# Optimization experiments

Measured on AMD Instinct MI355X. Metric: run time of the kernel, lower is better.

The kernel has to match this reference:

```python
import jax, jax.numpy as jnp
import numpy as np

D_MODEL = 1024
NUM_HEADS = 4
KEY_DIM = 1024      # expand_k = 1
VALUE_DIM = 2048    # expand_v = 2
HEAD_QK = KEY_DIM // NUM_HEADS   # 256
HEAD_V = VALUE_DIM // NUM_HEADS  # 512
EPS = 1e-5
CHUNK = 64
ROPE_BASE = 10000.0


def apply_rotary(q, k):
    # q, k: (b, n, h, d), non-interleaved (rotate-half) rotary
    n, d = q.shape[1], q.shape[-1]
    inv_freq = 1.0 / (ROPE_BASE ** (jnp.arange(0, d, 2, dtype=jnp.float32) / d))
    t = jnp.arange(n, dtype=jnp.float32)
    freqs = jnp.outer(t, inv_freq)                     # (n, d/2)
    cos = jnp.cos(freqs)[None, :, None, :]
    sin = jnp.sin(freqs)[None, :, None, :]
    def rot(x):
        x1, x2 = jnp.split(x, 2, axis=-1)
        return jnp.concatenate([x1 * cos - x2 * sin, x2 * cos + x1 * sin], axis=-1)
    return rot(q), rot(k)


def chunk_retention(q, k, v, gamma, chunk=CHUNK):
    # q,k: (B,H,N,dk); v: (B,H,N,dv); gamma: (H,) per-head decay
    B, H, N, dk = q.shape
    dv = v.shape[-1]
    NC = N // chunk
    # (NC, B, H, C, d) chunked layout for scan
    qc = jnp.moveaxis(q.reshape(B, H, NC, chunk, dk), 2, 0)
    kc = jnp.moveaxis(k.reshape(B, H, NC, chunk, dk), 2, 0)
    vc = jnp.moveaxis(v.reshape(B, H, NC, chunk, dv), 2, 0)

    idx = jnp.arange(chunk)
    rel = idx[:, None] - idx[None, :]                       # i - j
    # intra-chunk decay mask D[h,i,j] = gamma_h**(i-j) for i>=j else 0
    D = jnp.where(rel >= 0, gamma[:, None, None] ** rel, 0.0)       # (H,C,C)
    cross_q = (gamma[:, None] ** (idx + 1))[None, :, :, None]       # (1,H,C,1)
    cross_k = (gamma[:, None] ** (chunk - 1 - idx))[None, :, :, None]
    gC = (gamma ** chunk)[None, :, None, None]                      # (1,H,1,1)

    def step(S, qkv):
        qb, kb, vb = qkv                                    # (B,H,C,d)
        attn = jnp.einsum('bhid,bhjd->bhij', qb, kb) * D[None]
        o_intra = jnp.einsum('bhij,bhjd->bhid', attn, vb)
        o_inter = jnp.einsum('bhid,bhde->bhie', qb * cross_q, S)
        S_new = gC * S + jnp.einsum('bhjd,bhje->bhde', kb * cross_k, vb)
        return S_new, o_intra + o_inter

    S0 = jnp.zeros((B, H, dk, dv), dtype=q.dtype)
    _, o = jax.lax.scan(step, S0, (qc, kc, vc))             # (NC,B,H,C,dv)
    return jnp.moveaxis(o, 0, 2).reshape(B, H, N, dv)


def rmsnorm(x, w):
    var = jnp.mean(x * x, axis=-1, keepdims=True)
    return x * jax.lax.rsqrt(var + EPS) * w


def setup_inputs() -> dict:
    key = jax.random.key(0)
    ks = jax.random.split(key, 7)
    B, N = 2, 4096
    s = 0.02
    return {
        'x': jax.random.normal(ks[0], (B, N, D_MODEL), dtype=jnp.float32),
        'Wq': jax.random.normal(ks[1], (D_MODEL, D_MODEL), dtype=jnp.float32) * s,
        'Wk': jax.random.normal(ks[2], (D_MODEL, D_MODEL), dtype=jnp.float32) * s,
        'Wv': jax.random.normal(ks[3], (D_MODEL, VALUE_DIM), dtype=jnp.float32) * s,
        'Wg': jax.random.normal(ks[4], (D_MODEL, VALUE_DIM), dtype=jnp.float32) * s,
        'Wo': jax.random.normal(ks[5], (VALUE_DIM, D_MODEL), dtype=jnp.float32) * s,
        'gn_weight': jnp.ones((HEAD_V,), dtype=jnp.float32),
    }


def reference(x, Wq, Wk, Wv, Wg, Wo, gn_weight):
    B, N, _ = x.shape
    H = NUM_HEADS
    q1 = (x @ Wq).reshape(B, N, H, HEAD_QK)
    k1 = (x @ Wk).reshape(B, N, H, HEAD_QK)
    q1, k1 = apply_rotary(q1, k1)
    q = jnp.transpose(q1, (0, 2, 1, 3)) * (HEAD_QK ** -0.5)   # (B,H,N,dk)
    k = jnp.transpose(k1, (0, 2, 1, 3))
    v = jnp.transpose((x @ Wv).reshape(B, N, H, HEAD_V), (0, 2, 1, 3))
    gamma = 1.0 - jnp.exp2(-5.0 - jnp.arange(H, dtype=jnp.float32))
    o = chunk_retention(q, k, v, gamma)                       # (B,H,N,dv_h)
    o = jnp.transpose(o, (0, 2, 1, 3))                        # (B,N,H,dv_h)
    o = rmsnorm(o, gn_weight)
    g = jax.nn.silu(x @ Wg)                                   # (B,N,VALUE_DIM)
    o = o.reshape(B, N, VALUE_DIM) * g
    return o @ Wo
```

## Files before the change

kernel.cpp:

```cpp
#include <hip/hip_runtime.h>

#define NS   4096
#define NBAT 2
#define NH   4
#define DKH  256
#define DVH  512
#define DM   1024
#define VD   2048
#define CH   64
#define NCH  64
#define MROW (NBAT * NS)

typedef unsigned short u16;
typedef unsigned int   u32;

using bf16x8 = __attribute__((ext_vector_type(8))) short;
using bf16x4 = __attribute__((ext_vector_type(4))) short;
using f32x4  = __attribute__((ext_vector_type(4))) float;

__device__ __forceinline__ float bf2f(u16 a) {
  return __uint_as_float(((u32)a) << 16);
}
__device__ __forceinline__ u16 f2bf(float f) {
  u32 u = __float_as_uint(f);
  u32 r = (u + 0x7fffu + ((u >> 16) & 1u)) >> 16;
  return (u16)r;
}
__device__ __forceinline__ void unpack2(u32 v, float& lo, float& hi) {
  lo = __uint_as_float(v << 16);
  hi = __uint_as_float(v & 0xffff0000u);
}
__device__ __forceinline__ void unpack8(uint4 v, float* f) {
  unpack2(v.x, f[0], f[1]); unpack2(v.y, f[2], f[3]);
  unpack2(v.z, f[4], f[5]); unpack2(v.w, f[6], f[7]);
}

__device__ __forceinline__ void gl_lds16(const u16* g, u16* l) {
  __builtin_amdgcn_global_load_lds(
      (const __attribute__((address_space(1))) void*)g,
      (__attribute__((address_space(3))) void*)l,
      16, 0, 0);
}

__device__ __forceinline__ f32x4 mfma32(bf16x8 a, bf16x8 b, f32x4 c) {
  return __builtin_amdgcn_mfma_f32_16x16x32_bf16(a, b, c, 0, 0, 0);
}

__device__ __forceinline__ f32x4 mfma16(bf16x4 a, bf16x4 b, f32x4 c) {
#if __has_builtin(__builtin_amdgcn_mfma_f32_16x16x16bf16_1k)
  return __builtin_amdgcn_mfma_f32_16x16x16bf16_1k(a, b, c, 0, 0, 0);
#else
  asm("v_mfma_f32_16x16x16_bf16 %0, %1, %2, %0" : "+v"(c) : "v"(a), "v"(b));
  return c;
#endif
}

__device__ __forceinline__ bf16x8 scale8(bf16x8 v, const float* ckv) {
  u32* w = (u32*)&v;
  bf16x8 out;
  u32* ow = (u32*)&out;
#pragma unroll
  for (int p = 0; p < 4; p++) {
    float lo, hi; unpack2(w[p], lo, hi);
    ow[p] = (u32)f2bf(lo * ckv[2 * p]) | ((u32)f2bf(hi * ckv[2 * p + 1]) << 16);
  }
  return out;
}

__device__ __forceinline__ bf16x4 pack4(f32x4 v) {
  bf16x4 o;
  o[0] = (short)f2bf(v[0]); o[1] = (short)f2bf(v[1]);
  o[2] = (short)f2bf(v[2]); o[3] = (short)f2bf(v[3]);
  return o;
}

__global__ __launch_bounds__(256) void cvt_bf16(const float* __restrict__ X,
                                                u16* __restrict__ Y) {
  size_t t = (size_t)blockIdx.x * 256 + threadIdx.x;
  float4 v = *(const float4*)(X + t * 4);
  ushort4 o;
  o.x = f2bf(v.x); o.y = f2bf(v.y); o.z = f2bf(v.z); o.w = f2bf(v.w);
  *(ushort4*)(Y + t * 4) = o;
}

__global__ __launch_bounds__(256) void transpose_bf16(const float* __restrict__ W,
                                                      u16* __restrict__ Wt,
                                                      int K, int N) {
  __shared__ float tile[64][65];
  const int n0 = blockIdx.x * 64, k0 = blockIdx.y * 64;
  const int t = threadIdx.x;
  const int r = t >> 4, c = (t & 15) << 2;
#pragma unroll
  for (int it = 0; it < 4; it++) {
    float4 v = *(const float4*)(W + (size_t)(k0 + r + it * 16) * N + n0 + c);
    tile[r + it * 16][c + 0] = v.x; tile[r + it * 16][c + 1] = v.y;
    tile[r + it * 16][c + 2] = v.z; tile[r + it * 16][c + 3] = v.w;
  }
  __syncthreads();
#pragma unroll
  for (int it = 0; it < 4; it++) {
    const int nr = r + it * 16;
    ushort4 o;
    o.x = f2bf(tile[c + 0][nr]); o.y = f2bf(tile[c + 1][nr]);
    o.z = f2bf(tile[c + 2][nr]); o.w = f2bf(tile[c + 3][nr]);
    *(ushort4*)(Wt + (size_t)(n0 + nr) * K + k0 + c) = o;
  }
}

template<int OMODE>
__global__ __launch_bounds__(256) void gemm_mfma(const u16* __restrict__ A,
                                                 const u16* __restrict__ Bt,
                                                 void* __restrict__ C,
                                                 int M, int N, int K) {
  __shared__ u16 sA[128 * 64];
  __shared__ u16 sB[128 * 64];
  const int tid = threadIdx.x;
  const int wave = tid >> 6, lane = tid & 63;
  const int wm = (wave >> 1) << 6;
  const int wn = (wave & 1) << 6;
  const int row0 = blockIdx.y << 7, col0 = blockIdx.x << 7;

  const int srow = tid >> 3;
  const int sk   = (tid & 7) << 3;

  const u16* aRow = A + (size_t)(row0 + srow) * K + sk;
  const u16* bRow = Bt + (size_t)(col0 + srow) * K + sk;
  u16* sAp = sA + tid * 8;
  u16* sBp = sB + tid * 8;

  f32x4 acc[4][4] = {};

  const int fm = lane & 15;
  const int fk = (lane >> 4) << 3;
  const u16* sAf = sA + (wm + fm) * 64 + fk;
  const u16* sBf = sB + (wn + fm) * 64 + fk;

  for (int k0 = 0; k0 < K; k0 += 64) {
#pragma unroll
    for (int it = 0; it < 4; it++) {
      gl_lds16(aRow + (size_t)(it * 32) * K + k0, sAp + it * 2048);
      gl_lds16(bRow + (size_t)(it * 32) * K + k0, sBp + it * 2048);
    }
    __syncthreads();
#pragma unroll
    for (int kk = 0; kk < 64; kk += 32) {
      bf16x8 af[4], bfr[4];
#pragma unroll
      for (int mt = 0; mt < 4; mt++) af[mt] = *(const bf16x8*)(sAf + mt * 1024 + kk);
#pragma unroll
      for (int nt = 0; nt < 4; nt++) bfr[nt] = *(const bf16x8*)(sBf + nt * 1024 + kk);
#pragma unroll
      for (int mt = 0; mt < 4; mt++)
#pragma unroll
        for (int nt = 0; nt < 4; nt++)
          acc[mt][nt] = mfma32(af[mt], bfr[nt], acc[mt][nt]);
    }
    __syncthreads();
  }

  const int er = lane >> 4;
  const int ec = lane & 15;
#pragma unroll
  for (int mt = 0; mt < 4; mt++) {
#pragma unroll
    for (int nt = 0; nt < 4; nt++) {
      if constexpr (OMODE == 2) {
        ushort4 o;
        o.x = f2bf(acc[mt][nt][0]); o.y = f2bf(acc[mt][nt][1]);
        o.z = f2bf(acc[mt][nt][2]); o.w = f2bf(acc[mt][nt][3]);
        u16* dst = (u16*)C + (size_t)(col0 + wn + nt * 16 + ec) * M +
                   row0 + wm + mt * 16 + er * 4;
        *(ushort4*)dst = o;
      } else {
#pragma unroll
        for (int r = 0; r < 4; r++) {
          const size_t row = (size_t)row0 + wm + mt * 16 + er * 4 + r;
          const size_t col = (size_t)col0 + wn + nt * 16 + ec;
          if constexpr (OMODE == 1) ((u16*)C)[row * N + col] = f2bf(acc[mt][nt][r]);
          else                      ((float*)C)[row * N + col] = acc[mt][nt][r];
        }
      }
    }
  }
}

__global__ __launch_bounds__(256) void rope_kernel(u16* __restrict__ Q, u16* __restrict__ K) {
  size_t t = (size_t)blockIdx.x * 256 + threadIdx.x;
  int j = (int)(t & 127);
  int h = (int)((t >> 7) & 3);
  size_t bn = t >> 9;
  int n = (int)(bn & (NS - 1));
  float ang = (float)n * exp2f(-(float)j * (13.2877123795494f / 128.0f));
  float s, c;
  sincosf(ang, &s, &c);
  size_t base = bn * DM + (size_t)h * DKH + j;
  const float sc = 0.0625f;
  float q1 = bf2f(Q[base]), q2 = bf2f(Q[base + 128]);
  Q[base]       = f2bf((q1 * c - q2 * s) * sc);
  Q[base + 128] = f2bf((q2 * c + q1 * s) * sc);
  float k1 = bf2f(K[base]), k2 = bf2f(K[base + 128]);
  K[base]       = f2bf(k1 * c - k2 * s);
  K[base + 128] = f2bf(k2 * c + k1 * s);
}

__global__ __launch_bounds__(256) void transpose_k(const u16* __restrict__ Kb,
                                                   u16* __restrict__ KT) {
  __shared__ u16 tile[64][68];
  const int wg = blockIdx.x;
  const int dt = wg & 3, nt = (wg >> 2) & 63, h = (wg >> 8) & 3, b = wg >> 10;
  const int tid = threadIdx.x;
  const int r = tid >> 2, cb = (tid & 3) << 4;
  const u16* src = Kb + (size_t)(b * NS + nt * 64 + r) * DM + h * DKH + dt * 64 + cb;
  *(uint4*)&tile[r][cb]     = *(const uint4*)(src);
  *(uint4*)&tile[r][cb + 8] = *(const uint4*)(src + 8);
  __syncthreads();
  const int dr = tid >> 2, ncb = (tid & 3) << 4;
  u32 w[8];
#pragma unroll
  for (int u = 0; u < 8; u++)
    w[u] = (u32)tile[ncb + 2 * u][dr] | ((u32)tile[ncb + 2 * u + 1][dr] << 16);
  u16* dst = KT + ((size_t)((b * NH + h) * 256) + dt * 64 + dr) * NS + nt * 64 + ncb;
  *(uint4*)(dst)     = make_uint4(w[0], w[1], w[2], w[3]);
  *(uint4*)(dst + 8) = make_uint4(w[4], w[5], w[6], w[7]);
}

__global__ __launch_bounds__(256) void attn_mfma(const u16* __restrict__ Q,
                                                 const u16* __restrict__ Kb,
                                                 u16* __restrict__ At) {
  __shared__ u16 sQ[64][264];
  __shared__ u16 sK[64][264];
  const int wg = blockIdx.x;
  const int c = wg & 63, h = (wg >> 6) & 3, b = wg >> 8;
  const int n0 = c << 6;
  const int tid = threadIdx.x;
  const int wave = tid >> 6, lane = tid & 63;
  const int quad = lane >> 4, col = lane & 15;
  {
    const int r = tid >> 2, cb = (tid & 3) << 6;
    const u16* qsrc = Q  + (size_t)(b * NS + n0 + r) * DM + h * DKH + cb;
    const u16* ksrc = Kb + (size_t)(b * NS + n0 + r) * DM + h * DKH + cb;
#pragma unroll
    for (int u = 0; u < 8; u++) {
      *(uint4*)&sQ[r][cb + u * 8] = *(const uint4*)(qsrc + u * 8);
      *(uint4*)&sK[r][cb + u * 8] = *(const uint4*)(ksrc + u * 8);
    }
  }
  __syncthreads();
  const int i0 = wave << 4;
  f32x4 acc[4] = {};
#pragma unroll
  for (int ks = 0; ks < 256; ks += 32) {
    bf16x8 a = *(const bf16x8*)&sQ[i0 + col][ks + quad * 8];
#pragma unroll
    for (int nt = 0; nt < 4; nt++) {
      bf16x8 bb = *(const bf16x8*)&sK[nt * 16 + col][ks + quad * 8];
      acc[nt] = mfma32(a, bb, acc[nt]);
    }
  }
  const float l2g = log2f(1.0f - exp2f(-5.0f - (float)h));
  u16* dst = At + ((size_t)wg << 12);
#pragma unroll
  for (int nt = 0; nt < 4; nt++) {
    int j = nt * 16 + col;
#pragma unroll
    for (int rr = 0; rr < 4; rr++) {
      int i = i0 + quad * 4 + rr;
      int rel = i - j;
      float v = (rel >= 0) ? acc[nt][rr] * exp2f((float)rel * l2g) : 0.0f;
      dst[i * 64 + j] = f2bf(v);
    }
  }
}

__global__ __launch_bounds__(64) void state_pass(const u16* __restrict__ KT,
                                                 const u16* __restrict__ VT,
                                                 u16* __restrict__ Sc) {
  const int wg = blockIdx.x;
  const int bh = wg & 7, slice = wg >> 3;
  const int ds = slice & 7, es = slice >> 3;
  const int b = bh >> 2, h = bh & 3;
  const int lane = threadIdx.x;
  const int quad = lane >> 4, col = lane & 15;
  const float gamma = 1.0f - exp2f(-5.0f - (float)h);
  const float l2g = log2f(gamma);
  const float gC = exp2f(64.0f * l2g);
  float ck[2][8];
#pragma unroll
  for (int ks = 0; ks < 2; ks++)
#pragma unroll
    for (int u = 0; u < 8; u++)
      ck[ks][u] = exp2f((float)(63 - (ks * 32 + quad * 8 + u)) * l2g);

  const u16* KTb = KT + (size_t)(bh * 256 + ds * 32) * NS;
  const u16* vrow = VT + (size_t)(h * DVH + es * 16 + col) * MROW + (size_t)b * NS;

  f32x4 S[2] = {};
  bf16x8 kf[2][4], vf[2][2];

#pragma unroll
  for (int mt = 0; mt < 2; mt++)
#pragma unroll
    for (int ks = 0; ks < 2; ks++)
      kf[0][mt * 2 + ks] = *(const bf16x8*)(KTb + (size_t)(mt * 16 + col) * NS + ks * 32 + quad * 8);
#pragma unroll
  for (int ks = 0; ks < 2; ks++)
    vf[0][ks] = *(const bf16x8*)(vrow + ks * 32 + quad * 8);

#pragma unroll 2
  for (int ch = 0; ch < NCH; ch++) {
    const int cur = ch & 1, nxt = cur ^ 1;
    if (ch + 1 < NCH) {
      const int n1 = (ch + 1) << 6;
#pragma unroll
      for (int mt = 0; mt < 2; mt++)
#pragma unroll
        for (int ks = 0; ks < 2; ks++)
          kf[nxt][mt * 2 + ks] = *(const bf16x8*)(KTb + (size_t)(mt * 16 + col) * NS + n1 + ks * 32 + quad * 8);
#pragma unroll
      for (int ks = 0; ks < 2; ks++)
        vf[nxt][ks] = *(const bf16x8*)(vrow + n1 + ks * 32 + quad * 8);
    }
#pragma unroll
    for (int mt = 0; mt < 2; mt++) S[mt] *= gC;
#pragma unroll
    for (int ks = 0; ks < 2; ks++) {
      bf16x8 ckv = scale8(vf[cur][ks], ck[ks]);
#pragma unroll
      for (int mt = 0; mt < 2; mt++)
        S[mt] = mfma32(kf[cur][mt * 2 + ks], ckv, S[mt]);
    }
    if ((ch & 7) == 7 && ch != NCH - 1) {
      const int sidx = ch >> 3;
      u16* sp = Sc + (size_t)((bh * 7 + sidx) * 512 + es * 16 + col) * 256 + ds * 32;
#pragma unroll
      for (int mt = 0; mt < 2; mt++) {
        ushort4 o;
        o.x = f2bf(S[mt][0]); o.y = f2bf(S[mt][1]);
        o.z = f2bf(S[mt][2]); o.w = f2bf(S[mt][3]);
        *(ushort4*)(sp + mt * 16 + quad * 4) = o;
      }
    }
  }
}

__global__ __launch_bounds__(64, 1) void out_pass(const u16* __restrict__ Q,
                                                  const u16* __restrict__ KT,
                                                  const u16* __restrict__ At,
                                                  const u16* __restrict__ VT,
                                                  const u16* __restrict__ Sc,
                                                  u16* __restrict__ O) {
  const int wg = blockIdx.x;
  const int grp = wg & 63, es = wg >> 6;
  const int sc = grp & 7, bh = grp >> 3;
  const int b = bh >> 2, h = bh & 3;
  const int lane = threadIdx.x;
  const int quad = lane >> 4, col = lane & 15;
  const float gamma = 1.0f - exp2f(-5.0f - (float)h);
  const float l2g = log2f(gamma);
  const float gC = exp2f(64.0f * l2g);
  const float g16 = exp2f(16.0f * l2g);
  const float cq00 = exp2f((float)(quad * 4 + 1) * l2g);
  float ck[2][8];
#pragma unroll
  for (int ks = 0; ks < 2; ks++)
#pragma unroll
    for (int u = 0; u < 8; u++)
      ck[ks][u] = exp2f((float)(63 - (ks * 32 + quad * 8 + u)) * l2g);

  const u16* Qb  = Q + (size_t)(b * NS) * DM + h * DKH;
  const u16* KTb = KT + (size_t)(bh * 256) * NS;
  const u16* Atb = At + ((size_t)(bh * NCH) << 12);
  const u16* vrow0 = VT + (size_t)(h * DVH + es * 32 + col) * MROW + (size_t)b * NS;
  const u16* vrow1 = vrow0 + (size_t)16 * MROW;
  u16* Ob = O + (size_t)(b * NS) * VD + h * DVH + es * 32;

  f32x4 S[2][16];
  bf16x4 SB[2][16];
  if (sc) {
    const u16* sp0 = Sc + (size_t)((bh * 7 + sc - 1) * 512 + es * 32 + col) * 256;
    const u16* sp1 = sp0 + (size_t)16 * 256;
#pragma unroll
    for (int mt = 0; mt < 16; mt++) {
      ushort4 w0 = *(const ushort4*)(sp0 + mt * 16 + quad * 4);
      ushort4 w1 = *(const ushort4*)(sp1 + mt * 16 + quad * 4);
      SB[0][mt][0] = (short)w0.x; SB[0][mt][1] = (short)w0.y;
      SB[0][mt][2] = (short)w0.z; SB[0][mt][3] = (short)w0.w;
      SB[1][mt][0] = (short)w1.x; SB[1][mt][1] = (short)w1.y;
      SB[1][mt][2] = (short)w1.z; SB[1][mt][3] = (short)w1.w;
      S[0][mt] = f32x4{bf2f(w0.x), bf2f(w0.y), bf2f(w0.z), bf2f(w0.w)};
      S[1][mt] = f32x4{bf2f(w1.x), bf2f(w1.y), bf2f(w1.z), bf2f(w1.w)};
    }
  } else {
#pragma unroll
    for (int nt = 0; nt < 2; nt++)
#pragma unroll
      for (int mt = 0; mt < 16; mt++) { S[nt][mt] = f32x4{0.f, 0.f, 0.f, 0.f}; SB[nt][mt] = bf16x4{0, 0, 0, 0}; }
  }

  for (int c = 0; c < 8; c++) {
    const int ch = sc * 8 + c;
    const int n0 = ch << 6;
    f32x4 ai[4][2] = {}, ae[4][2] = {};
    bf16x8 vfr[2][2];
#pragma unroll
    for (int ks = 0; ks < 2; ks++) {
      vfr[ks][0] = *(const bf16x8*)(vrow0 + n0 + ks * 32 + quad * 8);
      vfr[ks][1] = *(const bf16x8*)(vrow1 + n0 + ks * 32 + quad * 8);
#pragma unroll
      for (int mt = 0; mt < 4; mt++) {
        bf16x8 a = *(const bf16x8*)(Atb + ((size_t)ch << 12) + (mt * 16 + col) * 64 + ks * 32 + quad * 8);
        ai[mt][0] = mfma32(a, vfr[ks][0], ai[mt][0]);
        ai[mt][1] = mfma32(a, vfr[ks][1], ai[mt][1]);
      }
    }
    if (sc || c) {
#pragma unroll
      for (int kt = 0; kt < 16; kt++) {
#pragma unroll
        for (int mt = 0; mt < 4; mt++) {
          ushort4 qa = *(const ushort4*)(Qb + (size_t)(n0 + mt * 16 + col) * DM + kt * 16 + quad * 4);
          bf16x4 a; a[0] = (short)qa.x; a[1] = (short)qa.y; a[2] = (short)qa.z; a[3] = (short)qa.w;
          ae[mt][0] = mfma16(a, SB[0][kt], ae[mt][0]);
          ae[mt][1] = mfma16(a, SB[1][kt], ae[mt][1]);
        }
      }
    }
    float cqr = cq00;
#pragma unroll
    for (int mt = 0; mt < 4; mt++) {
      float cq = cqr;
#pragma unroll
      for (int r = 0; r < 4; r++) {
        u16* dst = Ob + (size_t)(n0 + mt * 16 + quad * 4 + r) * VD;
        dst[col]      = f2bf(ai[mt][0][r] + cq * ae[mt][0][r]);
        dst[16 + col] = f2bf(ai[mt][1][r] + cq * ae[mt][1][r]);
        cq *= gamma;
      }
      cqr *= g16;
    }
    if (c < 7) {
#pragma unroll
      for (int nt = 0; nt < 2; nt++)
#pragma unroll
        for (int mt = 0; mt < 16; mt++) S[nt][mt] *= gC;
#pragma unroll
      for (int ks = 0; ks < 2; ks++) {
        bf16x8 ckv0 = scale8(vfr[ks][0], ck[ks]);
        bf16x8 ckv1 = scale8(vfr[ks][1], ck[ks]);
#pragma unroll
        for (int mt = 0; mt < 16; mt++) {
          bf16x8 a = *(const bf16x8*)(KTb + (size_t)(mt * 16 + col) * NS + n0 + ks * 32 + quad * 8);
          S[0][mt] = mfma32(a, ckv0, S[0][mt]);
          S[1][mt] = mfma32(a, ckv1, S[1][mt]);
        }
      }
#pragma unroll
      for (int nt = 0; nt < 2; nt++)
#pragma unroll
        for (int mt = 0; mt < 16; mt++) SB[nt][mt] = pack4(S[nt][mt]);
    }
  }
}

__global__ __launch_bounds__(256) void norm_gate_kernel(const u16* __restrict__ O,
                                                        const u16* __restrict__ G,
                                                        const float* __restrict__ gnw,
                                                        u16* __restrict__ OG) {
  const int bn = blockIdx.x;
  const int wave = threadIdx.x >> 6;
  const int lane = threadIdx.x & 63;
  const size_t base = (size_t)bn * VD + (size_t)wave * DVH;
  float vals[8];
  float ss = 0.f;
#pragma unroll
  for (int k = 0; k < 8; k++) {
    float v = bf2f(O[base + lane + 64 * k]);
    vals[k] = v;
    ss += v * v;
  }
#pragma unroll
  for (int off = 32; off > 0; off >>= 1) ss += __shfl_xor(ss, off, 64);
  const float r = rsqrtf(ss * (1.0f / 512.0f) + 1e-5f);
#pragma unroll
  for (int k = 0; k < 8; k++) {
    int e = lane + 64 * k;
    float g = bf2f(G[base + e]);
    float sig = 1.0f / (1.0f + expf(-g));
    OG[base + e] = f2bf(vals[k] * r * gnw[e] * g * sig);
  }
}

extern "C" void kernel_launch(void* const* d_in, const int* in_sizes, int n_in,
                              void* d_out, int out_size, void* d_ws, size_t ws_size,
                              hipStream_t stream) {
  const float* x   = (const float*)d_in[0];
  const float* Wq  = (const float*)d_in[1];
  const float* Wk  = (const float*)d_in[2];
  const float* Wv  = (const float*)d_in[3];
  const float* Wg  = (const float*)d_in[4];
  const float* Wo  = (const float*)d_in[5];
  const float* gnw = (const float*)d_in[6];

  char* ws = (char*)d_ws;
  u16*   xb  = (u16*)(ws);
  u16*   Sc  = (u16*)(ws);
  u16*   Qb  = (u16*)(ws + (16u  << 20));
  u16*   Kb  = (u16*)(ws + (32u  << 20));
  u16*   VT  = (u16*)(ws + (48u  << 20));
  u16*   Gb  = (u16*)(ws + (80u  << 20));
  u16*   At  = (u16*)(ws + (112u << 20));
  u16*   KTg = (u16*)(ws + (116u << 20));
  u16*   Wqt = (u16*)(ws + (132u << 20));
  u16*   Wkt = (u16*)(ws + (134u << 20));
  u16*   Wvt = (u16*)(ws + (136u << 20));
  u16*   Wgt = (u16*)(ws + (140u << 20));
  u16*   Wot = (u16*)(ws + (144u << 20));
  u16*   Ob  = (u16*)(ws + (148u << 20));
  u16*   OG  = (u16*)(ws);

  dim3 blk(256);
  const int M = MROW;

  cvt_bf16<<<8192, blk, 0, stream>>>(x, xb);
  transpose_bf16<<<dim3(16, 16), blk, 0, stream>>>(Wq, Wqt, DM, DM);
  transpose_bf16<<<dim3(16, 16), blk, 0, stream>>>(Wk, Wkt, DM, DM);
  transpose_bf16<<<dim3(32, 16), blk, 0, stream>>>(Wv, Wvt, DM, VD);
  transpose_bf16<<<dim3(32, 16), blk, 0, stream>>>(Wg, Wgt, DM, VD);
  transpose_bf16<<<dim3(16, 32), blk, 0, stream>>>(Wo, Wot, VD, DM);

  gemm_mfma<1><<<dim3(8, 64),  blk, 0, stream>>>(xb, Wqt, Qb, M, DM, DM);
  gemm_mfma<1><<<dim3(8, 64),  blk, 0, stream>>>(xb, Wkt, Kb, M, DM, DM);
  gemm_mfma<2><<<dim3(16, 64), blk, 0, stream>>>(xb, Wvt, VT, M, VD, DM);
  gemm_mfma<1><<<dim3(16, 64), blk, 0, stream>>>(xb, Wgt, Gb, M, VD, DM);

  rope_kernel<<<16384, blk, 0, stream>>>(Qb, Kb);
  transpose_k<<<2048, blk, 0, stream>>>(Kb, KTg);
  attn_mfma<<<512, blk, 0, stream>>>(Qb, Kb, At);

  state_pass<<<2048, dim3(64), 0, stream>>>(KTg, VT, Sc);
  out_pass<<<1024, dim3(64), 0, stream>>>(Qb, KTg, At, VT, Sc, Ob);

  norm_gate_kernel<<<M, blk, 0, stream>>>(Ob, Gb, gnw, OG);
  gemm_mfma<0><<<dim3(8, 64), blk, 0, stream>>>(OG, Wot, (float*)d_out, M, DM, VD);
}
```

Baseline: 668.8 us.

## Restructure out_pass to 4-wave blocks with LDS-staged state and K=32 MFMA

out_pass now runs 256-thread blocks where each wave owns a 16-column slice of the value dimension instead of 32 columns. The per-wave state operand is staged through LDS as bf16 so the inter-chunk product can use the 16x16x32 MFMA with 8-wide loads, replacing the 16x16x16 instruction and halving the register-resident state. state_pass also stops eight chunks early, since only the seven state checkpoints it writes are ever consumed. The aim is lower VGPR pressure and higher occupancy, at the cost of reloading Q, K and the At tile once per 16 columns rather than once per 32, plus LDS traffic.

```diff
diff --git a/kernel.cpp b/kernel.cpp
--- a/kernel.cpp
+++ b/kernel.cpp
@@ -15,7 +15,6 @@
 typedef unsigned int   u32;
 
 using bf16x8 = __attribute__((ext_vector_type(8))) short;
-using bf16x4 = __attribute__((ext_vector_type(4))) short;
 using f32x4  = __attribute__((ext_vector_type(4))) float;
 
 __device__ __forceinline__ float bf2f(u16 a) {
@@ -46,15 +45,6 @@
   return __builtin_amdgcn_mfma_f32_16x16x32_bf16(a, b, c, 0, 0, 0);
 }
 
-__device__ __forceinline__ f32x4 mfma16(bf16x4 a, bf16x4 b, f32x4 c) {
-#if __has_builtin(__builtin_amdgcn_mfma_f32_16x16x16bf16_1k)
-  return __builtin_amdgcn_mfma_f32_16x16x16bf16_1k(a, b, c, 0, 0, 0);
-#else
-  asm("v_mfma_f32_16x16x16_bf16 %0, %1, %2, %0" : "+v"(c) : "v"(a), "v"(b));
-  return c;
-#endif
-}
-
 __device__ __forceinline__ bf16x8 scale8(bf16x8 v, const float* ckv) {
   u32* w = (u32*)&v;
   bf16x8 out;
@@ -65,13 +55,6 @@
     ow[p] = (u32)f2bf(lo * ckv[2 * p]) | ((u32)f2bf(hi * ckv[2 * p + 1]) << 16);
   }
   return out;
-}
-
-__device__ __forceinline__ bf16x4 pack4(f32x4 v) {
-  bf16x4 o;
-  o[0] = (short)f2bf(v[0]); o[1] = (short)f2bf(v[1]);
-  o[2] = (short)f2bf(v[2]); o[3] = (short)f2bf(v[3]);
-  return o;
 }
 
 __global__ __launch_bounds__(256) void cvt_bf16(const float* __restrict__ X,
@@ -307,9 +290,9 @@
     vf[0][ks] = *(const bf16x8*)(vrow + ks * 32 + quad * 8);
 
 #pragma unroll 2
-  for (int ch = 0; ch < NCH; ch++) {
+  for (int ch = 0; ch < 56; ch++) {
     const int cur = ch & 1, nxt = cur ^ 1;
-    if (ch + 1 < NCH) {
+    if (ch + 1 < 56) {
       const int n1 = (ch + 1) << 6;
 #pragma unroll
       for (int mt = 0; mt < 2; mt++)
@@ -329,7 +312,7 @@
       for (int mt = 0; mt < 2; mt++)
         S[mt] = mfma32(kf[cur][mt * 2 + ks], ckv, S[mt]);
     }
-    if ((ch & 7) == 7 && ch != NCH - 1) {
+    if ((ch & 7) == 7) {
       const int sidx = ch >> 3;
       u16* sp = Sc + (size_t)((bh * 7 + sidx) * 512 + es * 16 + col) * 256 + ds * 32;
 #pragma unroll
@@ -343,18 +326,23 @@
   }
 }
 
-__global__ __launch_bounds__(64, 1) void out_pass(const u16* __restrict__ Q,
-                                                  const u16* __restrict__ KT,
-                                                  const u16* __restrict__ At,
-                                                  const u16* __restrict__ VT,
-                                                  const u16* __restrict__ Sc,
-                                                  u16* __restrict__ O) {
+__global__ __launch_bounds__(256) void out_pass(const u16* __restrict__ Q,
+                                                const u16* __restrict__ KT,
+                                                const u16* __restrict__ At,
+                                                const u16* __restrict__ VT,
+                                                const u16* __restrict__ Sc,
+                                                u16* __restrict__ O) {
+  __shared__ u16 sSb[4][16][264];
   const int wg = blockIdx.x;
-  const int grp = wg & 63, es = wg >> 6;
+  const int ev = wg >> 6, grp = wg & 63;
   const int sc = grp & 7, bh = grp >> 3;
   const int b = bh >> 2, h = bh & 3;
-  const int lane = threadIdx.x;
+  const int tid = threadIdx.x;
+  const int wv = tid >> 6, lane = tid & 63;
   const int quad = lane >> 4, col = lane & 15;
+  const int e0 = (ev * 4 + wv) << 4;
+  u16 (*mySb)[264] = sSb[wv];
+
   const float gamma = 1.0f - exp2f(-5.0f - (float)h);
   const float l2g = log2f(gamma);
   const float gC = exp2f(64.0f * l2g);
@@ -367,61 +355,53 @@
     for (int u = 0; u < 8; u++)
       ck[ks][u] = exp2f((float)(63 - (ks * 32 + quad * 8 + u)) * l2g);
 
-  const u16* Qb  = Q + (size_t)(b * NS) * DM + h * DKH;
-  const u16* KTb = KT + (size_t)(bh * 256) * NS;
-  const u16* Atb = At + ((size_t)(bh * NCH) << 12);
-  const u16* vrow0 = VT + (size_t)(h * DVH + es * 32 + col) * MROW + (size_t)b * NS;
-  const u16* vrow1 = vrow0 + (size_t)16 * MROW;
-  u16* Ob = O + (size_t)(b * NS) * VD + h * DVH + es * 32;
-
-  f32x4 S[2][16];
-  bf16x4 SB[2][16];
+  const u16* Qbh  = Q + (size_t)(b * NS) * DM + h * DKH;
+  const u16* KTbh = KT + (size_t)(bh * 256) * NS;
+  const u16* Atbh = At + ((size_t)(bh * NCH) << 12);
+  const u16* vrow = VT + (size_t)(h * DVH + e0 + col) * MROW + (size_t)b * NS;
+  u16* Obh = O + (size_t)(b * NS) * VD + h * DVH + e0;
+
+  f32x4 S[16];
   if (sc) {
-    const u16* sp0 = Sc + (size_t)((bh * 7 + sc - 1) * 512 + es * 32 + col) * 256;
-    const u16* sp1 = sp0 + (size_t)16 * 256;
+    const u16* sp = Sc + (size_t)((bh * 7 + sc - 1) * 512 + e0 + col) * 256;
 #pragma unroll
     for (int mt = 0; mt < 16; mt++) {
-      ushort4 w0 = *(const ushort4*)(sp0 + mt * 16 + quad * 4);
-      ushort4 w1 = *(const ushort4*)(sp1 + mt * 16 + quad * 4);
-      SB[0][mt][0] = (short)w0.x; SB[0][mt][1] = (short)w0.y;
-      SB[0][mt][2] = (short)w0.z; SB[0][mt][3] = (short)w0.w;
-      SB[1][mt][0] = (short)w1.x; SB[1][mt][1] = (short)w1.y;
-      SB[1][mt][2] = (short)w1.z; SB[1][mt][3] = (short)w1.w;
-      S[0][mt] = f32x4{bf2f(w0.x), bf2f(w0.y), bf2f(w0.z), bf2f(w0.w)};
-      S[1][mt] = f32x4{bf2f(w1.x), bf2f(w1.y), bf2f(w1.z), bf2f(w1.w)};
+      ushort4 w = *(const ushort4*)(sp + mt * 16 + quad * 4);
+      *(ushort4*)&mySb[col][mt * 16 + quad * 4] = w;
+      S[mt] = f32x4{bf2f(w.x), bf2f(w.y), bf2f(w.z), bf2f(w.w)};
     }
   } else {
-#pragma unroll
-    for (int nt = 0; nt < 2; nt++)
-#pragma unroll
-      for (int mt = 0; mt < 16; mt++) { S[nt][mt] = f32x4{0.f, 0.f, 0.f, 0.f}; SB[nt][mt] = bf16x4{0, 0, 0, 0}; }
+    const ushort4 z = {0, 0, 0, 0};
+#pragma unroll
+    for (int mt = 0; mt < 16; mt++) {
+      *(ushort4*)&mySb[col][mt * 16 + quad * 4] = z;
+      S[mt] = f32x4{0.f, 0.f, 0.f, 0.f};
+    }
   }
 
   for (int c = 0; c < 8; c++) {
     const int ch = sc * 8 + c;
     const int n0 = ch << 6;
-    f32x4 ai[4][2] = {}, ae[4][2] = {};
-    bf16x8 vfr[2][2];
-#pragma unroll
-    for (int ks = 0; ks < 2; ks++) {
-      vfr[ks][0] = *(const bf16x8*)(vrow0 + n0 + ks * 32 + quad * 8);
-      vfr[ks][1] = *(const bf16x8*)(vrow1 + n0 + ks * 32 + quad * 8);
+    bf16x8 vfr[2];
+    vfr[0] = *(const bf16x8*)(vrow + n0 + quad * 8);
+    vfr[1] = *(const bf16x8*)(vrow + n0 + 32 + quad * 8);
+    f32x4 ai[4] = {};
+#pragma unroll
+    for (int ks = 0; ks < 2; ks++)
 #pragma unroll
       for (int mt = 0; mt < 4; mt++) {
-        bf16x8 a = *(const bf16x8*)(Atb + ((size_t)ch << 12) + (mt * 16 + col) * 64 + ks * 32 + quad * 8);
-        ai[mt][0] = mfma32(a, vfr[ks][0], ai[mt][0]);
-        ai[mt][1] = mfma32(a, vfr[ks][1], ai[mt][1]);
-      }
-    }
-    if (sc || c) {
-#pragma unroll
-      for (int kt = 0; kt < 16; kt++) {
+        bf16x8 a = *(const bf16x8*)(Atbh + ((size_t)ch << 12) + (mt * 16 + col) * 64 + ks * 32 + quad * 8);
+        ai[mt] = mfma32(a, vfr[ks], ai[mt]);
+      }
+    f32x4 ae[4] = {};
+    if (ch) {
+#pragma unroll
+      for (int ks = 0; ks < 8; ks++) {
+        bf16x8 bb = *(const bf16x8*)&mySb[col][ks * 32 + quad * 8];
 #pragma unroll
         for (int mt = 0; mt < 4; mt++) {
-          ushort4 qa = *(const ushort4*)(Qb + (size_t)(n0 + mt * 16 + col) * DM + kt * 16 + quad * 4);
-          bf16x4 a; a[0] = (short)qa.x; a[1] = (short)qa.y; a[2] = (short)qa.z; a[3] = (short)qa.w;
-          ae[mt][0] = mfma16(a, SB[0][kt], ae[mt][0]);
-          ae[mt][1] = mfma16(a, SB[1][kt], ae[mt][1]);
+          bf16x8 a = *(const bf16x8*)(Qbh + (size_t)(n0 + mt * 16 + col) * DM + ks * 32 + quad * 8);
+          ae[mt] = mfma32(a, bb, ae[mt]);
         }
       }
     }
@@ -431,33 +411,31 @@
       float cq = cqr;
 #pragma unroll
       for (int r = 0; r < 4; r++) {
-        u16* dst = Ob + (size_t)(n0 + mt * 16 + quad * 4 + r) * VD;
-        dst[col]      = f2bf(ai[mt][0][r] + cq * ae[mt][0][r]);
-        dst[16 + col] = f2bf(ai[mt][1][r] + cq * ae[mt][1][r]);
+        u16* dst = Obh + (size_t)(n0 + mt * 16 + quad * 4 + r) * VD + col;
+        *dst = f2bf(ai[mt][r] + cq * ae[mt][r]);
         cq *= gamma;
       }
       cqr *= g16;
     }
     if (c < 7) {
 #pragma unroll
-      for (int nt = 0; nt < 2; nt++)
-#pragma unroll
-        for (int mt = 0; mt < 16; mt++) S[nt][mt] *= gC;
+      for (int mt = 0; mt < 16; mt++) S[mt] *= gC;
 #pragma unroll
       for (int ks = 0; ks < 2; ks++) {
-        bf16x8 ckv0 = scale8(vfr[ks][0], ck[ks]);
-        bf16x8 ckv1 = scale8(vfr[ks][1], ck[ks]);
+        bf16x8 ckv = scale8(vfr[ks], ck[ks]);
 #pragma unroll
         for (int mt = 0; mt < 16; mt++) {
-          bf16x8 a = *(const bf16x8*)(KTb + (size_t)(mt * 16 + col) * NS + n0 + ks * 32 + quad * 8);
-          S[0][mt] = mfma32(a, ckv0, S[0][mt]);
-          S[1][mt] = mfma32(a, ckv1, S[1][mt]);
+          bf16x8 a = *(const bf16x8*)(KTbh + (size_t)(mt * 16 + col) * NS + n0 + ks * 32 + quad * 8);
+          S[mt] = mfma32(a, ckv, S[mt]);
         }
       }
 #pragma unroll
-      for (int nt = 0; nt < 2; nt++)
-#pragma unroll
-        for (int mt = 0; mt < 16; mt++) SB[nt][mt] = pack4(S[nt][mt]);
+      for (int mt = 0; mt < 16; mt++) {
+        ushort4 o4;
+        o4.x = f2bf(S[mt][0]); o4.y = f2bf(S[mt][1]);
+        o4.z = f2bf(S[mt][2]); o4.w = f2bf(S[mt][3]);
+        *(ushort4*)&mySb[col][mt * 16 + quad * 4] = o4;
+      }
     }
   }
 }
@@ -538,7 +516,7 @@
   attn_mfma<<<512, blk, 0, stream>>>(Qb, Kb, At);
 
   state_pass<<<2048, dim3(64), 0, stream>>>(KTg, VT, Sc);
-  out_pass<<<1024, dim3(64), 0, stream>>>(Qb, KTg, At, VT, Sc, Ob);
+  out_pass<<<512, blk, 0, stream>>>(Qb, KTg, At, VT, Sc, Ob);
 
   norm_gate_kernel<<<M, blk, 0, stream>>>(Ob, Gb, gnw, OG);
   gemm_mfma<0><<<dim3(8, 64), blk, 0, stream>>>(OG, Wot, (float*)d_out, M, DM, VD);
```

Result: faster. 645.5 us (-3.5%).
